# Kernel optimization log

Measured on AMD Instinct MI355X. Metric: run time of the kernel, lower is better.

## Reference

```python
import jax, jax.numpy as jnp
import numpy as np
from jax import lax

B = 131072
STEPS = 50
HID = 64
NFEAT = 11
EPS = 1e-06
DT = 1.0 / 30.0


def setup_inputs() -> dict:
    key = jax.random.key(0)
    ks = jax.random.split(key, 10)
    # positions inside arena [20,780]x[20,580], velocities modest
    pos = jnp.concatenate([
        jax.random.uniform(ks[0], (B, STEPS, 1), minval=100.0, maxval=700.0),
        jax.random.uniform(ks[1], (B, STEPS, 1), minval=100.0, maxval=500.0),
        jax.random.uniform(ks[2], (B, STEPS, 1), minval=100.0, maxval=700.0),
        jax.random.uniform(ks[3], (B, STEPS, 1), minval=100.0, maxval=500.0),
    ], axis=-1)
    vel = jax.random.uniform(ks[4], (B, STEPS, 4), minval=-50.0, maxval=50.0)
    inputs = jnp.concatenate([pos, vel], axis=-1).astype(jnp.float32)
    s = 0.1
    W1 = (jax.random.normal(ks[5], (NFEAT, HID)) * s).astype(jnp.float32)
    b1 = jnp.zeros((HID,), jnp.float32)
    W2 = (jax.random.normal(ks[6], (HID, HID)) * s).astype(jnp.float32)
    b2 = jnp.zeros((HID,), jnp.float32)
    W3 = (jax.random.normal(ks[7], (HID, 2)) * s).astype(jnp.float32)
    b3 = jnp.zeros((2,), jnp.float32)
    gravity = jnp.array([-9.8], jnp.float32)
    friction_raw = jnp.array([0.1], jnp.float32)
    return {"inputs": inputs, "W1": W1, "b1": b1, "W2": W2, "b2": b2,
            "W3": W3, "b3": b3, "gravity": gravity, "friction_raw": friction_raw}


def _physics_features(state):
    # state: [B, 8]
    pos1, pos2 = state[:, 0:2], state[:, 2:4]
    vel1, vel2 = state[:, 4:6], state[:, 6:8]

    def polar(pos, vel):
        r = jnp.sqrt(jnp.sum(pos ** 2, axis=-1, keepdims=True))
        theta = jnp.arctan2(pos[:, 1:2], pos[:, 0:1])
        v_r = jnp.sum(pos * vel, axis=-1, keepdims=True) / (r + EPS)
        v_theta = (pos[:, 0:1] * vel[:, 1:2] - pos[:, 1:2] * vel[:, 0:1]) / (r ** 2 + EPS)
        L = r * v_theta
        return r, theta, v_r, v_theta, L

    r1, t1, vr1, vt1, L1 = polar(pos1, vel1)
    r2, t2, vr2, vt2, L2 = polar(pos2, vel2)
    r12 = jnp.sqrt(jnp.sum((pos2 - pos1) ** 2, axis=-1, keepdims=True))
    feats = jnp.concatenate([r1, t1, vr1, vt1, L1, r2, t2, vr2, vt2, L2, r12], axis=-1)
    return feats, pos1, pos2, vel1, vel2


def _bounce(new_pos, new_vel, hi_y):
    # reflect velocity with 0.8 restitution and clip position to arena
    mx = jnp.logical_or(new_pos[:, 0] < 20.0, new_pos[:, 0] > 780.0)
    vx = jnp.where(mx, -0.8 * new_vel[:, 0], new_vel[:, 0])
    px = jnp.clip(new_pos[:, 0], 20.0, 780.0)
    my = jnp.logical_or(new_pos[:, 1] < 20.0, new_pos[:, 1] > hi_y)
    vy = jnp.where(my, -0.8 * new_vel[:, 1], new_vel[:, 1])
    py = jnp.clip(new_pos[:, 1], 20.0, hi_y)
    return jnp.stack([px, py], axis=-1), jnp.stack([vx, vy], axis=-1)


def reference(inputs, W1, b1, W2, b2, W3, b3, gravity, friction_raw):
    steps = inputs.shape[1]
    friction = jnp.abs(friction_raw)          # [1]
    pixel_gravity = gravity[0] * 40.0          # scalar

    def step(state, _):
        feats, pos1, pos2, vel1, vel2 = _physics_features(state)
        # base acceleration: gravity (y only) minus friction drag
        g_vec = jnp.stack([jnp.zeros_like(pos1[:, 0]),
                           pixel_gravity * jnp.ones_like(pos1[:, 1])], axis=-1)
        acc1 = g_vec - friction * vel1
        acc2 = g_vec - friction * vel2
        # tiny correction MLP (note: same correction applied to both bodies,
        # matching original code which uses corrections[..., :2] twice)
        h = jnp.tanh(feats @ W1 + b1)
        h = jnp.tanh(h @ W2 + b2)
        corr = (h @ W3 + b3)[:, :2] * 0.1
        acc1 = acc1 + corr
        acc2 = acc2 + corr
        nv1 = vel1 + acc1 * DT
        nv2 = vel2 + acc2 * DT
        np1 = pos1 + nv1 * DT
        np2 = pos2 + nv2 * DT
        np1, nv1 = _bounce(np1, nv1, 580.0)
        np2, nv2 = _bounce(np2, nv2, 580.0)
        new_state = jnp.concatenate([np1, np2, nv1, nv2], axis=-1)
        return new_state, state

    _, states = lax.scan(step, inputs[:, 0, :], None, length=steps)
    return jnp.transpose(states, (1, 0, 2))  # [B, steps, 8]
```

## Files before the change

kernel.cpp:

```cpp
#include <hip/hip_runtime.h>
#include <math.h>

#define NSTEPS 50
#define NHID   64
#define NFEAT  11

__device__ __forceinline__ float fast_tanh(float x) {
    float e = __expf(x + x);
    return 1.0f - 2.0f * __builtin_amdgcn_rcpf(e + 1.0f);
}

__global__ __launch_bounds__(256, 2)
void phys_mlp_kernel(const float* __restrict__ inputs,
                     const float* __restrict__ W1,
                     const float* __restrict__ b1,
                     const float* __restrict__ W2,
                     const float* __restrict__ b2,
                     const float* __restrict__ W3,
                     const float* __restrict__ b3,
                     const float* __restrict__ grav,
                     const float* __restrict__ fric,
                     float* __restrict__ out,
                     int nb) {
    __shared__ __attribute__((aligned(16))) float sW2T[NHID * NHID];

    for (int i = threadIdx.x; i < NHID * NHID; i += 256)
        sW2T[i] = W2[((i & 63) << 6) | (i >> 6)];
    __syncthreads();

    int b = blockIdx.x * blockDim.x + threadIdx.x;
    if (b >= nb) return;

    const float DTF = 1.0f / 30.0f;
    float pg = __fmul_rn(grav[0], 40.0f);
    float fr = fabsf(fric[0]);

    const float4* in4 = (const float4*)(inputs + (size_t)b * NSTEPS * 8);
    float4 s0 = in4[0], s1 = in4[1];
    float p1x = s0.x, p1y = s0.y, p2x = s0.z, p2y = s0.w;
    float v1x = s1.x, v1y = s1.y, v2x = s1.z, v2y = s1.w;

    float4* o4 = (float4*)(out + (size_t)b * NSTEPS * 8);

    #pragma unroll 1
    for (int t = 0; t < NSTEPS; ++t) {
        o4[0] = make_float4(p1x, p1y, p2x, p2y);
        o4[1] = make_float4(v1x, v1y, v2x, v2y);
        o4 += 2;
        if (t == NSTEPS - 1) break;

        float feats[NFEAT];
        {
            float r = __fsqrt_rn(__fadd_rn(__fmul_rn(p1x, p1x), __fmul_rn(p1y, p1y)));
            feats[0] = r;
            feats[1] = atan2f(p1y, p1x);
            feats[2] = __fdiv_rn(__fadd_rn(__fmul_rn(p1x, v1x), __fmul_rn(p1y, v1y)),
                                 __fadd_rn(r, 1e-6f));
            float vt = __fdiv_rn(__fsub_rn(__fmul_rn(p1x, v1y), __fmul_rn(p1y, v1x)),
                                 __fadd_rn(__fmul_rn(r, r), 1e-6f));
            feats[3] = vt;
            feats[4] = __fmul_rn(r, vt);
        }
        {
            float r = __fsqrt_rn(__fadd_rn(__fmul_rn(p2x, p2x), __fmul_rn(p2y, p2y)));
            feats[5] = r;
            feats[6] = atan2f(p2y, p2x);
            feats[7] = __fdiv_rn(__fadd_rn(__fmul_rn(p2x, v2x), __fmul_rn(p2y, v2y)),
                                 __fadd_rn(r, 1e-6f));
            float vt = __fdiv_rn(__fsub_rn(__fmul_rn(p2x, v2y), __fmul_rn(p2y, v2x)),
                                 __fadd_rn(__fmul_rn(r, r), 1e-6f));
            feats[8] = vt;
            feats[9] = __fmul_rn(r, vt);
        }
        {
            float dx = __fsub_rn(p2x, p1x), dy = __fsub_rn(p2y, p1y);
            feats[10] = __fsqrt_rn(__fadd_rn(__fmul_rn(dx, dx), __fmul_rn(dy, dy)));
        }

        float h1[NHID];
        #pragma unroll
        for (int j = 0; j < NHID; ++j) h1[j] = b1[j];
        #pragma unroll
        for (int k = 0; k < NFEAT; ++k) {
            float f = feats[k];
            #pragma unroll
            for (int j = 0; j < NHID; ++j)
                h1[j] = fmaf(f, W1[k * NHID + j], h1[j]);
        }
        #pragma unroll
        for (int j = 0; j < NHID; ++j) h1[j] = fast_tanh(h1[j]);

        float c0 = b3[0], c1 = b3[1];
        #pragma unroll 1
        for (int j = 0; j < NHID; j += 4) {
            const float4* __restrict__ w0 = (const float4*)(sW2T + (j << 6));
            const float4* __restrict__ w1 = w0 + (NHID / 4);
            const float4* __restrict__ w2 = w1 + (NHID / 4);
            const float4* __restrict__ w3 = w2 + (NHID / 4);
            float a0 = b2[j], a1 = b2[j + 1], a2 = b2[j + 2], a3 = b2[j + 3];
            #pragma unroll
            for (int q = 0; q < NHID / 4; ++q) {
                float4 q0 = w0[q], q1 = w1[q], q2 = w2[q], q3 = w3[q];
                float h0 = h1[4 * q], hA = h1[4 * q + 1];
                float hB = h1[4 * q + 2], hC = h1[4 * q + 3];
                a0 = fmaf(h0, q0.x, a0); a0 = fmaf(hA, q0.y, a0);
                a0 = fmaf(hB, q0.z, a0); a0 = fmaf(hC, q0.w, a0);
                a1 = fmaf(h0, q1.x, a1); a1 = fmaf(hA, q1.y, a1);
                a1 = fmaf(hB, q1.z, a1); a1 = fmaf(hC, q1.w, a1);
                a2 = fmaf(h0, q2.x, a2); a2 = fmaf(hA, q2.y, a2);
                a2 = fmaf(hB, q2.z, a2); a2 = fmaf(hC, q2.w, a2);
                a3 = fmaf(h0, q3.x, a3); a3 = fmaf(hA, q3.y, a3);
                a3 = fmaf(hB, q3.z, a3); a3 = fmaf(hC, q3.w, a3);
            }
            float t0 = fast_tanh(a0), t1 = fast_tanh(a1);
            float t2 = fast_tanh(a2), t3 = fast_tanh(a3);
            c0 = fmaf(t0, W3[(j + 0) * 2], c0);  c1 = fmaf(t0, W3[(j + 0) * 2 + 1], c1);
            c0 = fmaf(t1, W3[(j + 1) * 2], c0);  c1 = fmaf(t1, W3[(j + 1) * 2 + 1], c1);
            c0 = fmaf(t2, W3[(j + 2) * 2], c0);  c1 = fmaf(t2, W3[(j + 2) * 2 + 1], c1);
            c0 = fmaf(t3, W3[(j + 3) * 2], c0);  c1 = fmaf(t3, W3[(j + 3) * 2 + 1], c1);
        }
        float corr0 = __fmul_rn(c0, 0.1f);
        float corr1 = __fmul_rn(c1, 0.1f);

        float ax1 = __fadd_rn(__fsub_rn(0.0f, __fmul_rn(fr, v1x)), corr0);
        float ay1 = __fadd_rn(__fsub_rn(pg,   __fmul_rn(fr, v1y)), corr1);
        float ax2 = __fadd_rn(__fsub_rn(0.0f, __fmul_rn(fr, v2x)), corr0);
        float ay2 = __fadd_rn(__fsub_rn(pg,   __fmul_rn(fr, v2y)), corr1);
        float nv1x = __fadd_rn(v1x, __fmul_rn(ax1, DTF));
        float nv1y = __fadd_rn(v1y, __fmul_rn(ay1, DTF));
        float nv2x = __fadd_rn(v2x, __fmul_rn(ax2, DTF));
        float nv2y = __fadd_rn(v2y, __fmul_rn(ay2, DTF));
        float np1x = __fadd_rn(p1x, __fmul_rn(nv1x, DTF));
        float np1y = __fadd_rn(p1y, __fmul_rn(nv1y, DTF));
        float np2x = __fadd_rn(p2x, __fmul_rn(nv2x, DTF));
        float np2y = __fadd_rn(p2y, __fmul_rn(nv2y, DTF));

        nv1x = (np1x < 20.0f || np1x > 780.0f) ? __fmul_rn(-0.8f, nv1x) : nv1x;
        np1x = fminf(fmaxf(np1x, 20.0f), 780.0f);
        nv1y = (np1y < 20.0f || np1y > 580.0f) ? __fmul_rn(-0.8f, nv1y) : nv1y;
        np1y = fminf(fmaxf(np1y, 20.0f), 580.0f);
        nv2x = (np2x < 20.0f || np2x > 780.0f) ? __fmul_rn(-0.8f, nv2x) : nv2x;
        np2x = fminf(fmaxf(np2x, 20.0f), 780.0f);
        nv2y = (np2y < 20.0f || np2y > 580.0f) ? __fmul_rn(-0.8f, nv2y) : nv2y;
        np2y = fminf(fmaxf(np2y, 20.0f), 580.0f);

        p1x = np1x; p1y = np1y; p2x = np2x; p2y = np2y;
        v1x = nv1x; v1y = nv1y; v2x = nv2x; v2y = nv2y;
    }
}

extern "C" void kernel_launch(void* const* d_in, const int* in_sizes, int n_in,
                              void* d_out, int out_size, void* d_ws, size_t ws_size,
                              hipStream_t stream) {
    const float* inputs = (const float*)d_in[0];
    const float* W1     = (const float*)d_in[1];
    const float* b1     = (const float*)d_in[2];
    const float* W2     = (const float*)d_in[3];
    const float* b2     = (const float*)d_in[4];
    const float* W3     = (const float*)d_in[5];
    const float* b3     = (const float*)d_in[6];
    const float* grav   = (const float*)d_in[7];
    const float* fric   = (const float*)d_in[8];
    float* out = (float*)d_out;
    (void)d_ws; (void)ws_size;

    int nb = in_sizes[0] / (NSTEPS * 8);
    int blocks = (nb + 255) / 256;
    phys_mlp_kernel<<<blocks, 256, 0, stream>>>(inputs, W1, b1, W2, b2, W3, b3,
                                                grav, fric, out, nb);
}
```

Measured before the change: 1.553 ms.

## Split each batch element across two lanes with DPP exchange of hidden activations

```diff
diff --git a/kernel.cpp b/kernel.cpp
--- a/kernel.cpp
+++ b/kernel.cpp
@@ -10,7 +10,12 @@
     return 1.0f - 2.0f * __builtin_amdgcn_rcpf(e + 1.0f);
 }
 
-__global__ __launch_bounds__(256, 2)
+__device__ __forceinline__ float dpp_xor1(float x) {
+    int r = __builtin_amdgcn_update_dpp(0, __float_as_int(x), 0xB1, 0xF, 0xF, true);
+    return __int_as_float(r);
+}
+
+__global__ __launch_bounds__(256, 4)
 void phys_mlp_kernel(const float* __restrict__ inputs,
                      const float* __restrict__ W1,
                      const float* __restrict__ b1,
@@ -22,14 +27,33 @@
                      const float* __restrict__ fric,
                      float* __restrict__ out,
                      int nb) {
-    __shared__ __attribute__((aligned(16))) float sW2T[NHID * NHID];
-
-    for (int i = threadIdx.x; i < NHID * NHID; i += 256)
-        sW2T[i] = W2[((i & 63) << 6) | (i >> 6)];
+    __shared__ __attribute__((aligned(16))) float sW2[NHID * NHID];
+    __shared__ __attribute__((aligned(16))) float sW1[NFEAT * NHID];
+    __shared__ __attribute__((aligned(16))) float sB1[NHID];
+    __shared__ __attribute__((aligned(16))) float sB2[NHID];
+
+    {
+        int tid = threadIdx.x;
+        for (int i = tid; i < NHID * NHID / 4; i += 256)
+            ((float4*)sW2)[i] = ((const float4*)W2)[i];
+        for (int i = tid; i < NFEAT * NHID / 4; i += 256)
+            ((float4*)sW1)[i] = ((const float4*)W1)[i];
+        if (tid < NHID / 4) ((float4*)sB1)[tid] = ((const float4*)b1)[tid];
+        else if (tid >= 64 && tid < 64 + NHID / 4)
+            ((float4*)sB2)[tid - 64] = ((const float4*)b2)[tid - 64];
+    }
     __syncthreads();
 
-    int b = blockIdx.x * blockDim.x + threadIdx.x;
+    int gtid = blockIdx.x * 256 + threadIdx.x;
+    int b = gtid >> 1;
     if (b >= nb) return;
+    const int  half = threadIdx.x & 1;
+    const bool odd  = (half != 0);
+
+    const float* myW1 = sW1 + (half << 5);
+    const float* myW2 = sW2 + (half << 5);
+    const float* myB1 = sB1 + (half << 5);
+    const float* myB2 = sB2 + (half << 5);
 
     const float DTF = 1.0f / 30.0f;
     float pg = __fmul_rn(grav[0], 40.0f);
@@ -40,13 +64,13 @@
     float p1x = s0.x, p1y = s0.y, p2x = s0.z, p2y = s0.w;
     float v1x = s1.x, v1y = s1.y, v2x = s1.z, v2y = s1.w;
 
-    float4* o4 = (float4*)(out + (size_t)b * NSTEPS * 8);
+    float* op = out + (size_t)b * NSTEPS * 8 + (half << 2);
 
     #pragma unroll 1
     for (int t = 0; t < NSTEPS; ++t) {
-        o4[0] = make_float4(p1x, p1y, p2x, p2y);
-        o4[1] = make_float4(v1x, v1y, v2x, v2y);
-        o4 += 2;
+        *(float4*)op = odd ? make_float4(v1x, v1y, v2x, v2y)
+                           : make_float4(p1x, p1y, p2x, p2y);
+        op += 8;
         if (t == NSTEPS - 1) break;
 
         float feats[NFEAT];
@@ -77,47 +101,62 @@
             feats[10] = __fsqrt_rn(__fadd_rn(__fmul_rn(dx, dx), __fmul_rn(dy, dy)));
         }
 
-        float h1[NHID];
-        #pragma unroll
-        for (int j = 0; j < NHID; ++j) h1[j] = b1[j];
+        float acc[32];
+        #pragma unroll
+        for (int q = 0; q < 8; ++q) {
+            float4 bq = *(const float4*)(myB1 + 4 * q);
+            acc[4 * q + 0] = bq.x; acc[4 * q + 1] = bq.y;
+            acc[4 * q + 2] = bq.z; acc[4 * q + 3] = bq.w;
+        }
         #pragma unroll
         for (int k = 0; k < NFEAT; ++k) {
             float f = feats[k];
             #pragma unroll
-            for (int j = 0; j < NHID; ++j)
-                h1[j] = fmaf(f, W1[k * NHID + j], h1[j]);
-        }
-        #pragma unroll
-        for (int j = 0; j < NHID; ++j) h1[j] = fast_tanh(h1[j]);
+            for (int q = 0; q < 8; ++q) {
+                float4 w = *(const float4*)(myW1 + k * NHID + 4 * q);
+                acc[4 * q + 0] = fmaf(f, w.x, acc[4 * q + 0]);
+                acc[4 * q + 1] = fmaf(f, w.y, acc[4 * q + 1]);
+                acc[4 * q + 2] = fmaf(f, w.z, acc[4 * q + 2]);
+                acc[4 * q + 3] = fmaf(f, w.w, acc[4 * q + 3]);
+            }
+        }
+        float h[32];
+        #pragma unroll
+        for (int j = 0; j < 32; ++j) h[j] = fast_tanh(acc[j]);
+
+        float a2[32];
+        #pragma unroll
+        for (int q = 0; q < 8; ++q) {
+            float4 bq = *(const float4*)(myB2 + 4 * q);
+            a2[4 * q + 0] = bq.x; a2[4 * q + 1] = bq.y;
+            a2[4 * q + 2] = bq.z; a2[4 * q + 3] = bq.w;
+        }
+        #pragma unroll
+        for (int k = 0; k < NHID; ++k) {
+            float own = h[k & 31];
+            float oth = dpp_xor1(own);
+            float hk  = (k < 32) ? (odd ? oth : own) : (odd ? own : oth);
+            #pragma unroll
+            for (int q = 0; q < 8; ++q) {
+                float4 w = *(const float4*)(myW2 + k * NHID + 4 * q);
+                a2[4 * q + 0] = fmaf(hk, w.x, a2[4 * q + 0]);
+                a2[4 * q + 1] = fmaf(hk, w.y, a2[4 * q + 1]);
+                a2[4 * q + 2] = fmaf(hk, w.z, a2[4 * q + 2]);
+                a2[4 * q + 3] = fmaf(hk, w.w, a2[4 * q + 3]);
+            }
+        }
+        float tt[32];
+        #pragma unroll
+        for (int j = 0; j < 32; ++j) tt[j] = fast_tanh(a2[j]);
 
         float c0 = b3[0], c1 = b3[1];
-        #pragma unroll 1
-        for (int j = 0; j < NHID; j += 4) {
-            const float4* __restrict__ w0 = (const float4*)(sW2T + (j << 6));
-            const float4* __restrict__ w1 = w0 + (NHID / 4);
-            const float4* __restrict__ w2 = w1 + (NHID / 4);
-            const float4* __restrict__ w3 = w2 + (NHID / 4);
-            float a0 = b2[j], a1 = b2[j + 1], a2 = b2[j + 2], a3 = b2[j + 3];
-            #pragma unroll
-            for (int q = 0; q < NHID / 4; ++q) {
-                float4 q0 = w0[q], q1 = w1[q], q2 = w2[q], q3 = w3[q];
-                float h0 = h1[4 * q], hA = h1[4 * q + 1];
-                float hB = h1[4 * q + 2], hC = h1[4 * q + 3];
-                a0 = fmaf(h0, q0.x, a0); a0 = fmaf(hA, q0.y, a0);
-                a0 = fmaf(hB, q0.z, a0); a0 = fmaf(hC, q0.w, a0);
-                a1 = fmaf(h0, q1.x, a1); a1 = fmaf(hA, q1.y, a1);
-                a1 = fmaf(hB, q1.z, a1); a1 = fmaf(hC, q1.w, a1);
-                a2 = fmaf(h0, q2.x, a2); a2 = fmaf(hA, q2.y, a2);
-                a2 = fmaf(hB, q2.z, a2); a2 = fmaf(hC, q2.w, a2);
-                a3 = fmaf(h0, q3.x, a3); a3 = fmaf(hA, q3.y, a3);
-                a3 = fmaf(hB, q3.z, a3); a3 = fmaf(hC, q3.w, a3);
-            }
-            float t0 = fast_tanh(a0), t1 = fast_tanh(a1);
-            float t2 = fast_tanh(a2), t3 = fast_tanh(a3);
-            c0 = fmaf(t0, W3[(j + 0) * 2], c0);  c1 = fmaf(t0, W3[(j + 0) * 2 + 1], c1);
-            c0 = fmaf(t1, W3[(j + 1) * 2], c0);  c1 = fmaf(t1, W3[(j + 1) * 2 + 1], c1);
-            c0 = fmaf(t2, W3[(j + 2) * 2], c0);  c1 = fmaf(t2, W3[(j + 2) * 2 + 1], c1);
-            c0 = fmaf(t3, W3[(j + 3) * 2], c0);  c1 = fmaf(t3, W3[(j + 3) * 2 + 1], c1);
+        #pragma unroll
+        for (int j = 0; j < NHID; ++j) {
+            float own = tt[j & 31];
+            float oth = dpp_xor1(own);
+            float tj  = (j < 32) ? (odd ? oth : own) : (odd ? own : oth);
+            c0 = fmaf(tj, W3[2 * j],     c0);
+            c1 = fmaf(tj, W3[2 * j + 1], c1);
         }
         float corr0 = __fmul_rn(c0, 0.1f);
         float corr1 = __fmul_rn(c1, 0.1f);
@@ -165,7 +204,8 @@
     (void)d_ws; (void)ws_size;
 
     int nb = in_sizes[0] / (NSTEPS * 8);
-    int blocks = (nb + 255) / 256;
+    int nthreads = nb * 2;
+    int blocks = (nthreads + 255) / 256;
     phys_mlp_kernel<<<blocks, 256, 0, stream>>>(inputs, W1, b1, W2, b2, W3, b3,
                                                 grav, fric, out, nb);
 }
```

New measurement: 3.566 ms. 2.3x slower.
